# Kernel optimization log

Hardware: AMD Instinct MI355X
Metric: run time of the kernel (lower is better)

Reference implementation:

```python
import jax, jax.numpy as jnp
import numpy as np

B_SZ, L, D_MODEL = 4, 4096, 512
D_INNER, N_HEADS, HEAD_DIM = 1024, 16, 64
D_STATE, D_CONV, CHUNK = 64, 4, 64
EPS = 1e-5


def setup_inputs() -> dict:
    key = jax.random.key(0)
    ks = jax.random.split(key, 12)
    return {
        'x': jax.random.normal(ks[0], (B_SZ, L, D_MODEL), jnp.float32),
        'W_in': jax.random.normal(ks[1], (D_MODEL, 2 * D_INNER), jnp.float32) * 0.02,
        'conv_x_kernel': jax.random.normal(ks[2], (D_CONV, 1, D_INNER), jnp.float32) * 0.1,
        'conv_x_bias': jnp.zeros((D_INNER,), jnp.float32),
        'conv_z_kernel': jax.random.normal(ks[3], (D_CONV, 1, D_INNER), jnp.float32) * 0.1,
        'conv_z_bias': jnp.zeros((D_INNER,), jnp.float32),
        'W_xdbl': jax.random.normal(ks[4], (D_INNER, N_HEADS + 2 * D_STATE), jnp.float32) * 0.02,
        'dt_bias': jax.random.normal(ks[5], (N_HEADS,), jnp.float32) * 0.5,
        'A_log': jax.random.uniform(ks[6], (N_HEADS,), jnp.float32, 0.0, 1.0),
        'D': jnp.ones((N_HEADS,), jnp.float32),
        'norm_weight': jnp.ones((D_INNER,), jnp.float32),
        'W_out': jax.random.normal(ks[7], (D_INNER, D_MODEL), jnp.float32) * 0.02,
    }


def dwconv(x, kernel, bias):
    # x: (b, l, d); kernel: (k, 1, d) depthwise, flax 'SAME' padding
    out = jax.lax.conv_general_dilated(
        x, kernel, window_strides=(1,), padding='SAME',
        dimension_numbers=('NWC', 'WIO', 'NWC'),
        feature_group_count=x.shape[-1])
    return out + bias


def segsum(a):
    # stable segment-sum: out[..., d, e] = sum_{e < i <= d} a[..., i]; -inf above diag
    T = a.shape[-1]
    a_rep = jnp.broadcast_to(a[..., :, None], a.shape + (T,))
    strict = jnp.tril(jnp.ones((T, T), bool), -1)
    seg = jnp.cumsum(jnp.where(strict, a_rep, 0.0), axis=-2)
    return jnp.where(jnp.tril(jnp.ones((T, T), bool)), seg, -jnp.inf)


def ssd(x, A, B, C, chunk):
    # x: (b,l,h,p), A: (b,l,h), B/C: (b,l,n) (single group, broadcast over heads)
    b, l, h, p = x.shape
    c = l // chunk
    x = x.reshape(b, c, chunk, h, p)
    A = A.reshape(b, c, chunk, h).transpose(0, 3, 1, 2)  # (b,h,c,l)
    B = B.reshape(b, c, chunk, -1)
    C = C.reshape(b, c, chunk, -1)
    A_cum = jnp.cumsum(A, axis=-1)
    Lmat = jnp.exp(segsum(A))  # (b,h,c,l,l)
    Y_diag = jnp.einsum('bcln,bcsn,bhcls,bcshp->bclhp', C, B, Lmat, x)
    decay_states = jnp.exp(A_cum[..., -1:] - A_cum)
    states = jnp.einsum('bcln,bhcl,bclhp->bchpn', B, decay_states, x)
    states = jnp.concatenate([jnp.zeros_like(states[:, :1]), states], axis=1)
    A_last = jnp.pad(A_cum[..., -1], ((0, 0), (0, 0), (1, 0)))
    decay_chunk = jnp.exp(segsum(A_last))  # (b,h,c+1,c+1)
    new_states = jnp.einsum('bhzc,bchpn->bzhpn', decay_chunk, states)
    states, final_state = new_states[:, :-1], new_states[:, -1]
    Y_off = jnp.einsum('bcln,bchpn,bhcl->bclhp', C, states, jnp.exp(A_cum))
    Y = (Y_diag + Y_off).reshape(b, l, h, p)
    return Y, final_state


def reference(x, W_in, conv_x_kernel, conv_x_bias, conv_z_kernel, conv_z_bias,
              W_xdbl, dt_bias, A_log, D, norm_weight, W_out):
    b, l, _ = x.shape
    xz = x @ W_in
    xi, z = jnp.split(xz, 2, axis=-1)
    xi = jax.nn.silu(dwconv(xi, conv_x_kernel, conv_x_bias))
    z = jax.nn.silu(dwconv(z, conv_z_kernel, conv_z_bias))
    x_dbl = xi @ W_xdbl  # (b,l,h+2n)
    dt = x_dbl[..., :N_HEADS]
    Bmat = x_dbl[..., N_HEADS:N_HEADS + D_STATE]
    Cmat = x_dbl[..., N_HEADS + D_STATE:]
    dt = jax.nn.softplus(dt + dt_bias)  # (b,l,h)
    A = -jnp.exp(A_log)  # (h,)
    xh = xi.reshape(b, l, N_HEADS, HEAD_DIM)
    y, _ = ssd(xh * dt[..., None], A * dt, Bmat, Cmat, CHUNK)
    y = y + xh * D[..., None]
    y = y.reshape(b, l, D_INNER)
    # gated RMSNorm (Mamba2 style): gate with silu(z), then rmsnorm with weight
    y = y * jax.nn.silu(z)
    y = y * jax.lax.rsqrt(jnp.mean(y * y, axis=-1, keepdims=True) + EPS) * norm_weight
    return y @ W_out
```

## Files before the change

### kernel.cpp

```cpp
#include <hip/hip_runtime.h>
#include <hip/hip_bf16.h>
#include <cstdint>

#define B_SZn 4
#define SEQ_L 4096
#define D_MODELn 512
#define D_INNERn 1024
#define N_HEADSn 16
#define HEAD_DIMn 64
#define D_STATEn 64
#define CHUNKn 64
#define NCHUNK (SEQ_L / CHUNKn)
#define BL (B_SZn * SEQ_L)
#define XDBL_N (N_HEADSn + 2 * D_STATEn)

typedef __hip_bfloat16 bf16;
typedef __bf16 bf16x8 __attribute__((ext_vector_type(8)));
typedef float f32x4 __attribute__((ext_vector_type(4)));

__device__ __forceinline__ float silu_f(float v) {
    return v / (1.0f + expf(-v));
}
__device__ __forceinline__ float b2f(unsigned short u) {
    return __uint_as_float((unsigned)u << 16);
}
__device__ __forceinline__ unsigned short f2b(float f) {
    bf16 h = __float2bfloat16(f);
    return *(unsigned short*)&h;
}
__device__ __forceinline__ void stf(float* p, float v) { *p = v; }
__device__ __forceinline__ void stf(bf16* p, float v) { *p = __float2bfloat16(v); }

__device__ __forceinline__ float4 us4_to_f4(ushort4 u) {
    float4 f;
    f.x = b2f(u.x); f.y = b2f(u.y); f.z = b2f(u.z); f.w = b2f(u.w);
    return f;
}

__device__ __forceinline__ void async_copy16(void* lds, const void* g) {
    __builtin_amdgcn_global_load_lds(
        (const __attribute__((address_space(1))) unsigned int*)g,
        (__attribute__((address_space(3))) unsigned int*)lds, 16, 0, 0);
}

__global__ __launch_bounds__(256) void cvt_f32_bf16(
    const float* __restrict__ in, bf16* __restrict__ out) {
    const int idx = blockIdx.x * 256 + threadIdx.x;
    float4 v = *(const float4*)(in + (size_t)idx * 4);
    ushort4 o;
    o.x = f2b(v.x); o.y = f2b(v.y); o.z = f2b(v.z); o.w = f2b(v.w);
    *(ushort4*)((unsigned short*)out + (size_t)idx * 4) = o;
}

__global__ __launch_bounds__(256) void transpose_cvt(
    const float* __restrict__ in, bf16* __restrict__ out, int R, int C) {
    __shared__ float t[32][33];
    const int bc = blockIdx.x * 32, br = blockIdx.y * 32;
    const int tx = threadIdx.x & 31, ty = threadIdx.x >> 5;
#pragma unroll
    for (int i = ty; i < 32; i += 8) {
        int r = br + i, c = bc + tx;
        t[i][tx] = (r < R && c < C) ? in[(size_t)r * C + c] : 0.f;
    }
    __syncthreads();
#pragma unroll
    for (int i = ty; i < 32; i += 8) {
        int c = bc + i, r = br + tx;
        if (c < C && r < R) out[(size_t)c * R + r] = __float2bfloat16(t[tx][i]);
    }
}

template <typename TO>
__global__ __launch_bounds__(256) void gemm_mfma(
    const bf16* __restrict__ A, const bf16* __restrict__ Bt,
    TO* __restrict__ C, int M, int N, int K) {
    __shared__ __align__(16) unsigned short Al[2][128 * 32];
    __shared__ __align__(16) unsigned short Bl[2][128 * 32];
    const int tid = threadIdx.x;
    const int wave = tid >> 6, lane = tid & 63;
    const int wm = (wave >> 1) * 64, wn = (wave & 1) * 64;
    int lin = blockIdx.y * gridDim.x + blockIdx.x;
    const int nwg = gridDim.x * gridDim.y;
    if ((nwg & 7) == 0) lin = (lin & 7) * (nwg >> 3) + (lin >> 3);
    const int bm = (lin / gridDim.x) * 128, bn = (lin % gridDim.x) * 128;
    f32x4 acc[4][4];
#pragma unroll
    for (int m = 0; m < 4; ++m)
#pragma unroll
        for (int n = 0; n < 4; ++n) acc[m][n] = (f32x4)(0.f);

    const int lrow = lane & 15, lk8 = (lane >> 4) * 8;
    const int srow = tid >> 2, sc8 = (tid & 3) * 8;
    for (int k0 = 0; k0 < K; k0 += 64) {
#pragma unroll
        for (int h = 0; h < 2; ++h) {
            const int kh = k0 + h * 32;
            async_copy16((char*)&Al[h][0] + (size_t)(wave * 64) * 16,
                         A + (size_t)(bm + srow) * K + kh + sc8);
            async_copy16((char*)&Al[h][0] + (size_t)(256 + wave * 64) * 16,
                         A + (size_t)(bm + 64 + srow) * K + kh + sc8);
            async_copy16((char*)&Bl[h][0] + (size_t)(wave * 64) * 16,
                         Bt + (size_t)(bn + srow) * K + kh + sc8);
            async_copy16((char*)&Bl[h][0] + (size_t)(256 + wave * 64) * 16,
                         Bt + (size_t)(bn + 64 + srow) * K + kh + sc8);
        }
        __syncthreads();
#pragma unroll
        for (int h = 0; h < 2; ++h) {
            bf16x8 af[4], bfr[4];
#pragma unroll
            for (int m = 0; m < 4; ++m)
                af[m] = *(const bf16x8*)(&Al[h][(wm + m * 16 + lrow) * 32 + lk8]);
#pragma unroll
            for (int n = 0; n < 4; ++n)
                bfr[n] = *(const bf16x8*)(&Bl[h][(wn + n * 16 + lrow) * 32 + lk8]);
#pragma unroll
            for (int m = 0; m < 4; ++m)
#pragma unroll
                for (int n = 0; n < 4; ++n)
                    acc[m][n] = __builtin_amdgcn_mfma_f32_16x16x32_bf16(
                        af[m], bfr[n], acc[m][n], 0, 0, 0);
        }
        __syncthreads();
    }
#pragma unroll
    for (int m = 0; m < 4; ++m) {
#pragma unroll
        for (int n = 0; n < 4; ++n) {
#pragma unroll
            for (int r = 0; r < 4; ++r) {
                int row = bm + wm + m * 16 + (lane >> 4) * 4 + r;
                int col = bn + wn + n * 16 + (lane & 15);
                if (row < M && col < N)
                    stf(&C[(size_t)row * N + col], acc[m][n][r]);
            }
        }
    }
}

__global__ __launch_bounds__(256) void conv_silu_kernel(
    const bf16* __restrict__ xz,
    const float* __restrict__ kx, const float* __restrict__ bx,
    const float* __restrict__ kz, const float* __restrict__ bz,
    bf16* __restrict__ xi, bf16* __restrict__ zo) {
    const int tid = threadIdx.x;
    const int d4 = tid * 4;
    const int blk = blockIdx.x;
    const int l0 = (blk * 8) & (SEQ_L - 1);
    const int b = (blk * 8) >> 12;
    const unsigned short* base = (const unsigned short*)xz +
                                 ((size_t)b * SEQ_L) * (2 * D_INNERn);
    float4 wx[4], wz[4];
#pragma unroll
    for (int k = 0; k < 4; ++k) {
        wx[k] = *(const float4*)(kx + k * D_INNERn + d4);
        wz[k] = *(const float4*)(kz + k * D_INNERn + d4);
    }
    const float4 bxv = *(const float4*)(bx + d4);
    const float4 bzv = *(const float4*)(bz + d4);
    float4 vx[4], vz[4];
#pragma unroll
    for (int j = 0; j < 3; ++j) {
        int l = l0 - 1 + j;
        if (l >= 0) {
            const unsigned short* row = base + (size_t)l * (2 * D_INNERn);
            vx[j] = us4_to_f4(*(const ushort4*)(row + d4));
            vz[j] = us4_to_f4(*(const ushort4*)(row + D_INNERn + d4));
        } else {
            vx[j] = make_float4(0.f, 0.f, 0.f, 0.f);
            vz[j] = make_float4(0.f, 0.f, 0.f, 0.f);
        }
    }
    unsigned short* xout = (unsigned short*)xi;
    unsigned short* zout = (unsigned short*)zo;
#pragma unroll
    for (int j = 0; j < 8; ++j) {
        const int lread = l0 + 2 + j;
        if (lread < SEQ_L) {
            const unsigned short* row = base + (size_t)lread * (2 * D_INNERn);
            vx[3] = us4_to_f4(*(const ushort4*)(row + d4));
            vz[3] = us4_to_f4(*(const ushort4*)(row + D_INNERn + d4));
        } else {
            vx[3] = make_float4(0.f, 0.f, 0.f, 0.f);
            vz[3] = make_float4(0.f, 0.f, 0.f, 0.f);
        }
        float4 ax = bxv, az = bzv;
#pragma unroll
        for (int k = 0; k < 4; ++k) {
            ax.x += vx[k].x * wx[k].x; ax.y += vx[k].y * wx[k].y;
            ax.z += vx[k].z * wx[k].z; ax.w += vx[k].w * wx[k].w;
            az.x += vz[k].x * wz[k].x; az.y += vz[k].y * wz[k].y;
            az.z += vz[k].z * wz[k].z; az.w += vz[k].w * wz[k].w;
        }
        ushort4 ox, oz;
        ox.x = f2b(silu_f(ax.x)); ox.y = f2b(silu_f(ax.y));
        ox.z = f2b(silu_f(ax.z)); ox.w = f2b(silu_f(ax.w));
        oz.x = f2b(silu_f(az.x)); oz.y = f2b(silu_f(az.y));
        oz.z = f2b(silu_f(az.z)); oz.w = f2b(silu_f(az.w));
        const size_t obase = ((size_t)b * SEQ_L + l0 + j) * D_INNERn + d4;
        *(ushort4*)(xout + obase) = ox;
        *(ushort4*)(zout + obase) = oz;
        vx[0] = vx[1]; vx[1] = vx[2]; vx[2] = vx[3];
        vz[0] = vz[1]; vz[1] = vz[2]; vz[2] = vz[3];
    }
}

__global__ __launch_bounds__(256) void dt_kernel(
    const unsigned short* __restrict__ xdbl, const float* __restrict__ dt_bias,
    float* __restrict__ dtp) {
    const int idx = blockIdx.x * 256 + threadIdx.x;
    const int h = idx & 15;
    const int r = idx >> 4;
    float v = b2f(xdbl[(size_t)r * XDBL_N + h]) + dt_bias[h];
    dtp[idx] = (v > 20.f) ? v : log1pf(expf(v));
}

__global__ __launch_bounds__(256) void ssd_chunk_mfma(
    const unsigned short* __restrict__ xdbl, const bf16* __restrict__ xi,
    const float* __restrict__ dtp, const float* __restrict__ A_log,
    const float* __restrict__ Dvec,
    unsigned short* __restrict__ y, unsigned short* __restrict__ S,
    float* __restrict__ acum_g, float* __restrict__ rchunk) {
    __shared__ __align__(16) unsigned short sBb[64 * 72];
    __shared__ __align__(16) unsigned short sCb[64 * 72];
    __shared__ __align__(16) unsigned short sXT[64 * 72];
    __shared__ __align__(16) unsigned short sGb[64 * 72];
    __shared__ __align__(16) unsigned short sWB[64 * 72];
    __shared__ float sdtp[64], sacum[64], sw[64];
    const int bid = blockIdx.x;
    const int h = bid & 15;
    const int bc = bid >> 4;
    const int c = bc & (NCHUNK - 1);
    const int b = bc >> 6;
    const int tid = threadIdx.x;
    const int wave = tid >> 6, lane = tid & 63;
    const int lrow = lane & 15, lk8 = (lane >> 4) * 8;
    const int row0 = b * SEQ_L + c * CHUNKn;
    const float Ah = -expf(A_log[h]);
    const float Dh = Dvec[h];

    if (tid < 64) sdtp[tid] = dtp[(size_t)(row0 + tid) * N_HEADSn + h];
    const unsigned short* xius = (const unsigned short*)xi;
#pragma unroll
    for (int it = 0; it < 16; ++it) {
        int e = tid + it * 256;
        int s = e >> 6, n = e & 63;
        const unsigned short* xr = xdbl + (size_t)(row0 + s) * XDBL_N + N_HEADSn;
        sBb[s * 72 + n] = xr[n];
        sCb[s * 72 + n] = xr[D_STATEn + n];
        sXT[n * 72 + s] = xius[(size_t)(row0 + s) * D_INNERn + h * HEAD_DIMn + n];
    }
    __syncthreads();
    if (wave == 0) {
        float v = Ah * sdtp[lane];
#pragma unroll
        for (int o = 1; o < 64; o <<= 1) {
            float t = __shfl_up(v, o);
            if (lane >= o) v += t;
        }
        sacum[lane] = v;
        float last = __shfl(v, 63);
        sw[lane] = expf(last - v) * sdtp[lane];
        acum_g[(size_t)bid * 64 + lane] = v;
        if (lane == 63) rchunk[bid] = expf(v);
    }
    f32x4 acc1[4];
#pragma unroll
    for (int t = 0; t < 4; ++t) acc1[t] = (f32x4)(0.f);
#pragma unroll
    for (int ks = 0; ks < 2; ++ks) {
        bf16x8 a = *(const bf16x8*)(&sCb[(wave * 16 + lrow) * 72 + ks * 32 + lk8]);
#pragma unroll
        for (int t = 0; t < 4; ++t) {
            bf16x8 bb = *(const bf16x8*)(&sBb[(t * 16 + lrow) * 72 + ks * 32 + lk8]);
            acc1[t] = __builtin_amdgcn_mfma_f32_16x16x32_bf16(a, bb, acc1[t], 0, 0, 0);
        }
    }
    __syncthreads();
#pragma unroll
    for (int t = 0; t < 4; ++t) {
#pragma unroll
        for (int r = 0; r < 4; ++r) {
            int l = wave * 16 + (lane >> 4) * 4 + r;
            int s = t * 16 + lrow;
            float val = 0.f;
            if (l >= s) val = acc1[t][r] * expf(sacum[l] - sacum[s]) * sdtp[s];
            sGb[l * 72 + s] = f2b(val);
        }
    }
#pragma unroll
    for (int it = 0; it < 16; ++it) {
        int e = tid + it * 256;
        int s = e >> 6, n = e & 63;
        sWB[n * 72 + s] = f2b(sw[s] * b2f(sBb[s * 72 + n]));
    }
    __syncthreads();
    f32x4 acc2[4], acc3[4];
#pragma unroll
    for (int t = 0; t < 4; ++t) { acc2[t] = (f32x4)(0.f); acc3[t] = (f32x4)(0.f); }
#pragma unroll
    for (int ks = 0; ks < 2; ++ks) {
        bf16x8 a2 = *(const bf16x8*)(&sGb[(wave * 16 + lrow) * 72 + ks * 32 + lk8]);
        bf16x8 a3 = *(const bf16x8*)(&sXT[(wave * 16 + lrow) * 72 + ks * 32 + lk8]);
#pragma unroll
        for (int t = 0; t < 4; ++t) {
            bf16x8 b2v = *(const bf16x8*)(&sXT[(t * 16 + lrow) * 72 + ks * 32 + lk8]);
            bf16x8 b3v = *(const bf16x8*)(&sWB[(t * 16 + lrow) * 72 + ks * 32 + lk8]);
            acc2[t] = __builtin_amdgcn_mfma_f32_16x16x32_bf16(a2, b2v, acc2[t], 0, 0, 0);
            acc3[t] = __builtin_amdgcn_mfma_f32_16x16x32_bf16(a3, b3v, acc3[t], 0, 0, 0);
        }
    }
#pragma unroll
    for (int t = 0; t < 4; ++t) {
#pragma unroll
        for (int r = 0; r < 4; ++r) {
            int rr = wave * 16 + (lane >> 4) * 4 + r;
            int cc = t * 16 + lrow;
            float xv = b2f(sXT[cc * 72 + rr]);
            y[(size_t)(row0 + rr) * D_INNERn + h * HEAD_DIMn + cc] =
                f2b(acc2[t][r] + Dh * xv);
            S[(size_t)bid * 4096 + rr * 64 + cc] = f2b(acc3[t][r]);
        }
    }
}

__global__ __launch_bounds__(256) void chunk_scan_kernel(
    unsigned short* __restrict__ S, const float* __restrict__ rchunk) {
    const int idx = blockIdx.x * 256 + threadIdx.x;
    const int pn2 = (idx & 2047) * 2;
    const int bh = idx >> 11;
    const int h = bh & 15;
    const int b = bh >> 4;
    float P0 = 0.f, P1 = 0.f;
    for (int c = 0; c < NCHUNK; ++c) {
        int bid = (b * NCHUNK + c) * N_HEADSn + h;
        size_t off = (size_t)bid * 4096 + pn2;
        unsigned int v = *(unsigned int*)(S + off);
        float s0 = b2f((unsigned short)(v & 0xffff));
        float s1 = b2f((unsigned short)(v >> 16));
        *(unsigned int*)(S + off) =
            (unsigned int)f2b(P0) | ((unsigned int)f2b(P1) << 16);
        float rc = rchunk[bid];
        P0 = rc * P0 + s0;
        P1 = rc * P1 + s1;
    }
}

__global__ __launch_bounds__(256) void yoff_mfma(
    const unsigned short* __restrict__ xdbl, const unsigned short* __restrict__ S,
    const float* __restrict__ acum_g, unsigned short* __restrict__ y) {
    __shared__ __align__(16) unsigned short sCb[64 * 72];
    __shared__ __align__(16) unsigned short sP[64 * 72];
    __shared__ float se[64];
    const int bid = blockIdx.x;
    const int h = bid & 15;
    const int bc = bid >> 4;
    const int c = bc & (NCHUNK - 1);
    const int b = bc >> 6;
    const int tid = threadIdx.x;
    const int wave = tid >> 6, lane = tid & 63;
    const int lrow = lane & 15, lk8 = (lane >> 4) * 8;
    const int row0 = b * SEQ_L + c * CHUNKn;
    if (tid < 64) se[tid] = expf(acum_g[(size_t)bid * 64 + tid]);
#pragma unroll
    for (int it = 0; it < 16; ++it) {
        int e = tid + it * 256;
        int r = e >> 6, n = e & 63;
        sCb[r * 72 + n] = xdbl[(size_t)(row0 + r) * XDBL_N + N_HEADSn + D_STATEn + n];
        sP[r * 72 + n] = S[(size_t)bid * 4096 + e];
    }
    __syncthreads();
    f32x4 acc[4];
#pragma unroll
    for (int t = 0; t < 4; ++t) acc[t] = (f32x4)(0.f);
#pragma unroll
    for (int ks = 0; ks < 2; ++ks) {
        bf16x8 a = *(const bf16x8*)(&sCb[(wave * 16 + lrow) * 72 + ks * 32 + lk8]);
#pragma unroll
        for (int t = 0; t < 4; ++t) {
            bf16x8 bb = *(const bf16x8*)(&sP[(t * 16 + lrow) * 72 + ks * 32 + lk8]);
            acc[t] = __builtin_amdgcn_mfma_f32_16x16x32_bf16(a, bb, acc[t], 0, 0, 0);
        }
    }
#pragma unroll
    for (int t = 0; t < 4; ++t) {
#pragma unroll
        for (int r = 0; r < 4; ++r) {
            int l = wave * 16 + (lane >> 4) * 4 + r;
            int p = t * 16 + lrow;
            size_t idx = (size_t)(row0 + l) * D_INNERn + h * HEAD_DIMn + p;
            y[idx] = f2b(b2f(y[idx]) + acc[t][r] * se[l]);
        }
    }
}

__global__ __launch_bounds__(256) void gate_norm_kernel(
    const unsigned short* __restrict__ y, const bf16* __restrict__ zb,
    const float* __restrict__ nw, bf16* __restrict__ y_bf) {
    const int row = blockIdx.x;
    const int tid = threadIdx.x;
    const size_t base = (size_t)row * D_INNERn + tid * 4;
    ushort4 yu = *(const ushort4*)(y + base);
    ushort4 zu = *(const ushort4*)((const unsigned short*)zb + base);
    float v0 = b2f(yu.x) * silu_f(b2f(zu.x));
    float v1 = b2f(yu.y) * silu_f(b2f(zu.y));
    float v2 = b2f(yu.z) * silu_f(b2f(zu.z));
    float v3 = b2f(yu.w) * silu_f(b2f(zu.w));
    float ss = v0 * v0 + v1 * v1 + v2 * v2 + v3 * v3;
#pragma unroll
    for (int o = 32; o > 0; o >>= 1) ss += __shfl_xor(ss, o);
    __shared__ float sred[4];
    if ((tid & 63) == 0) sred[tid >> 6] = ss;
    __syncthreads();
    float total = sred[0] + sred[1] + sred[2] + sred[3];
    float scale = rsqrtf(total * (1.0f / D_INNERn) + 1e-5f);
    float4 wv = *(const float4*)(nw + tid * 4);
    ushort4 o4;
    o4.x = f2b(v0 * scale * wv.x);
    o4.y = f2b(v1 * scale * wv.y);
    o4.z = f2b(v2 * scale * wv.z);
    o4.w = f2b(v3 * scale * wv.w);
    *(ushort4*)((unsigned short*)y_bf + base) = o4;
}

extern "C" void kernel_launch(void* const* d_in, const int* in_sizes, int n_in,
                              void* d_out, int out_size, void* d_ws, size_t ws_size,
                              hipStream_t stream) {
    (void)in_sizes; (void)n_in; (void)out_size; (void)ws_size;
    const float* x       = (const float*)d_in[0];
    const float* W_in    = (const float*)d_in[1];
    const float* ckx     = (const float*)d_in[2];
    const float* cbx     = (const float*)d_in[3];
    const float* ckz     = (const float*)d_in[4];
    const float* cbz     = (const float*)d_in[5];
    const float* W_xdbl  = (const float*)d_in[6];
    const float* dt_bias = (const float*)d_in[7];
    const float* A_log   = (const float*)d_in[8];
    const float* Dvec    = (const float*)d_in[9];
    const float* nw      = (const float*)d_in[10];
    const float* W_out   = (const float*)d_in[11];
    float* out = (float*)d_out;
    char* w = (char*)d_ws;

    bf16*  xz     = (bf16*)(w);
    unsigned short* y = (unsigned short*)(w);
    bf16*  xi     = (bf16*)(w + 67108864);
    bf16*  zb     = (bf16*)(w + 100663296);
    char*  Sreg   = w + 134217728;
    unsigned short* S = (unsigned short*)Sreg;
    bf16*  x_bf   = (bf16*)Sreg;
    bf16*  W_in_T = (bf16*)(Sreg + 16777216);
    bf16*  W_xd_T = (bf16*)(Sreg + 18874368);
    bf16*  y_bf   = (bf16*)Sreg;
    bf16*  W_o_T  = (bf16*)(Sreg + 33554432);
    unsigned short* xdbl = (unsigned short*)(w + 201326592);
    float* dtp    = (float*)(w + 210763776);
    float* acum   = (float*)(w + 211812352);
    float* rchunk = (float*)(w + 212860928);

    cvt_f32_bf16<<<BL * D_MODELn / 1024, 256, 0, stream>>>(x, x_bf);
    transpose_cvt<<<dim3(2048 / 32, 512 / 32), 256, 0, stream>>>(W_in, W_in_T, 512, 2048);
    transpose_cvt<<<dim3(5, 1024 / 32), 256, 0, stream>>>(W_xdbl, W_xd_T, 1024, 144);
    gemm_mfma<bf16><<<dim3(2048 / 128, BL / 128), 256, 0, stream>>>(
        x_bf, W_in_T, xz, BL, 2048, D_MODELn);
    conv_silu_kernel<<<BL / 8, 256, 0, stream>>>(xz, ckx, cbx, ckz, cbz, xi, zb);
    gemm_mfma<bf16><<<dim3(2, BL / 128), 256, 0, stream>>>(
        xi, W_xd_T, (bf16*)xdbl, BL, XDBL_N, D_INNERn);
    dt_kernel<<<BL * N_HEADSn / 256, 256, 0, stream>>>(xdbl, dt_bias, dtp);
    ssd_chunk_mfma<<<B_SZn * NCHUNK * N_HEADSn, 256, 0, stream>>>(
        xdbl, xi, dtp, A_log, Dvec, y, S, acum, rchunk);
    chunk_scan_kernel<<<B_SZn * N_HEADSn * 2048 / 256, 256, 0, stream>>>(S, rchunk);
    yoff_mfma<<<B_SZn * NCHUNK * N_HEADSn, 256, 0, stream>>>(xdbl, S, acum, y);
    transpose_cvt<<<dim3(512 / 32, 1024 / 32), 256, 0, stream>>>(W_out, W_o_T, 1024, 512);
    gate_norm_kernel<<<BL, 256, 0, stream>>>(y, zb, nw, y_bf);
    gemm_mfma<float><<<dim3(512 / 128, BL / 128), 256, 0, stream>>>(
        y_bf, W_o_T, out, BL, D_MODELn, D_INNERn);
}
```

Before: 257.8 us.

## Add wide 128x256 GEMM for in-proj, fuse dt softplus into SSD, set MFMA priority

The input projection GEMM switches to a new 512-thread kernel with 128x256 tiles, a grouped block-order remap and two-stage K staging. This is meant to improve B-tile reuse and L2 locality. The separate dt softplus kernel is removed and its work is recomputed inside ssd_chunk_mfma, which saves a launch and the dtp round trip through memory. s_setprio is raised around the MFMA loops in the SSD kernels so matrix work gets scheduling priority. The wider tile means fewer workgroups and more registers per wave, which may reduce occupancy.

```diff
diff --git a/kernel.cpp b/kernel.cpp
--- a/kernel.cpp
+++ b/kernel.cpp
@@ -138,6 +138,72 @@
     }
 }
 
+template <typename TO>
+__global__ __launch_bounds__(512) void gemm_mfma_wide(
+    const bf16* __restrict__ A, const bf16* __restrict__ Bt,
+    TO* __restrict__ C, int M, int N, int K) {
+    __shared__ __align__(16) unsigned short Al[2][128 * 32];
+    __shared__ __align__(16) unsigned short Bl[2][256 * 32];
+    const int tid = threadIdx.x;
+    const int wave = tid >> 6, lane = tid & 63;
+    const int wm = (wave >> 2) * 64, wn = (wave & 3) * 64;
+    int lin = blockIdx.y * gridDim.x + blockIdx.x;
+    const int nwg = gridDim.x * gridDim.y;
+    if ((nwg & 7) == 0) lin = (lin & 7) * (nwg >> 3) + (lin >> 3);
+    const int bm = (lin / gridDim.x) * 128, bn = (lin % gridDim.x) * 256;
+    f32x4 acc[4][4];
+#pragma unroll
+    for (int m = 0; m < 4; ++m)
+#pragma unroll
+        for (int n = 0; n < 4; ++n) acc[m][n] = (f32x4)(0.f);
+
+    const int lrow = lane & 15, lk8 = (lane >> 4) * 8;
+    const int srow = tid >> 2, sc8 = (tid & 3) * 8;
+    for (int k0 = 0; k0 < K; k0 += 64) {
+#pragma unroll
+        for (int h = 0; h < 2; ++h) {
+            const int kh = k0 + h * 32;
+            async_copy16((char*)&Al[h][0] + (size_t)(wave * 64) * 16,
+                         A + (size_t)(bm + srow) * K + kh + sc8);
+            async_copy16((char*)&Bl[h][0] + (size_t)(wave * 64) * 16,
+                         Bt + (size_t)(bn + srow) * K + kh + sc8);
+            async_copy16((char*)&Bl[h][0] + (size_t)(512 + wave * 64) * 16,
+                         Bt + (size_t)(bn + 128 + srow) * K + kh + sc8);
+        }
+        __syncthreads();
+#pragma unroll
+        for (int h = 0; h < 2; ++h) {
+            bf16x8 af[4], bfr[4];
+#pragma unroll
+            for (int m = 0; m < 4; ++m)
+                af[m] = *(const bf16x8*)(&Al[h][(wm + m * 16 + lrow) * 32 + lk8]);
+#pragma unroll
+            for (int n = 0; n < 4; ++n)
+                bfr[n] = *(const bf16x8*)(&Bl[h][(wn + n * 16 + lrow) * 32 + lk8]);
+#pragma unroll
+            for (int m = 0; m < 4; ++m)
+#pragma unroll
+                for (int n = 0; n < 4; ++n)
+                    acc[m][n] = __builtin_amdgcn_mfma_f32_16x16x32_bf16(
+                        af[m], bfr[n], acc[m][n], 0, 0, 0);
+        }
+        __syncthreads();
+    }
+#pragma unroll
+    for (int m = 0; m < 4; ++m) {
+#pragma unroll
+        for (int n = 0; n < 4; ++n) {
+#pragma unroll
+            for (int r = 0; r < 4; ++r) {
+                int row = bm + wm + m * 16 + (lane >> 4) * 4 + r;
+                int col = bn + wn + n * 16 + (lane & 15);
+                if (row < M && col < N)
+                    stf(&C[(size_t)row * N + col], acc[m][n][r]);
+            }
+        }
+    }
+}
+
 __global__ __launch_bounds__(256) void conv_silu_kernel(
     const bf16* __restrict__ xz,
     const float* __restrict__ kx, const float* __restrict__ bx,
@@ -205,19 +271,9 @@
     }
 }
 
-__global__ __launch_bounds__(256) void dt_kernel(
-    const unsigned short* __restrict__ xdbl, const float* __restrict__ dt_bias,
-    float* __restrict__ dtp) {
-    const int idx = blockIdx.x * 256 + threadIdx.x;
-    const int h = idx & 15;
-    const int r = idx >> 4;
-    float v = b2f(xdbl[(size_t)r * XDBL_N + h]) + dt_bias[h];
-    dtp[idx] = (v > 20.f) ? v : log1pf(expf(v));
-}
-
 __global__ __launch_bounds__(256) void ssd_chunk_mfma(
     const unsigned short* __restrict__ xdbl, const bf16* __restrict__ xi,
-    const float* __restrict__ dtp, const float* __restrict__ A_log,
+    const float* __restrict__ dt_bias, const float* __restrict__ A_log,
     const float* __restrict__ Dvec,
     unsigned short* __restrict__ y, unsigned short* __restrict__ S,
     float* __restrict__ acum_g, float* __restrict__ rchunk) {
@@ -239,7 +295,10 @@
     const float Ah = -expf(A_log[h]);
     const float Dh = Dvec[h];
 
-    if (tid < 64) sdtp[tid] = dtp[(size_t)(row0 + tid) * N_HEADSn + h];
+    if (tid < 64) {
+        float v = b2f(xdbl[(size_t)(row0 + tid) * XDBL_N + h]) + dt_bias[h];
+        sdtp[tid] = (v > 20.f) ? v : log1pf(expf(v));
+    }
     const unsigned short* xius = (const unsigned short*)xi;
 #pragma unroll
     for (int it = 0; it < 16; ++it) {
@@ -267,6 +326,7 @@
     f32x4 acc1[4];
 #pragma unroll
     for (int t = 0; t < 4; ++t) acc1[t] = (f32x4)(0.f);
+    __builtin_amdgcn_s_setprio(1);
 #pragma unroll
     for (int ks = 0; ks < 2; ++ks) {
         bf16x8 a = *(const bf16x8*)(&sCb[(wave * 16 + lrow) * 72 + ks * 32 + lk8]);
@@ -276,6 +336,7 @@
             acc1[t] = __builtin_amdgcn_mfma_f32_16x16x32_bf16(a, bb, acc1[t], 0, 0, 0);
         }
     }
+    __builtin_amdgcn_s_setprio(0);
     __syncthreads();
 #pragma unroll
     for (int t = 0; t < 4; ++t) {
@@ -298,6 +359,7 @@
     f32x4 acc2[4], acc3[4];
 #pragma unroll
     for (int t = 0; t < 4; ++t) { acc2[t] = (f32x4)(0.f); acc3[t] = (f32x4)(0.f); }
+    __builtin_amdgcn_s_setprio(1);
 #pragma unroll
     for (int ks = 0; ks < 2; ++ks) {
         bf16x8 a2 = *(const bf16x8*)(&sGb[(wave * 16 + lrow) * 72 + ks * 32 + lk8]);
@@ -310,6 +372,7 @@
             acc3[t] = __builtin_amdgcn_mfma_f32_16x16x32_bf16(a3, b3v, acc3[t], 0, 0, 0);
         }
     }
+    __builtin_amdgcn_s_setprio(0);
 #pragma unroll
     for (int t = 0; t < 4; ++t) {
 #pragma unroll
@@ -373,6 +436,7 @@
     f32x4 acc[4];
 #pragma unroll
     for (int t = 0; t < 4; ++t) acc[t] = (f32x4)(0.f);
+    __builtin_amdgcn_s_setprio(1);
 #pragma unroll
     for (int ks = 0; ks < 2; ++ks) {
         bf16x8 a = *(const bf16x8*)(&sCb[(wave * 16 + lrow) * 72 + ks * 32 + lk8]);
@@ -382,6 +446,7 @@
             acc[t] = __builtin_amdgcn_mfma_f32_16x16x32_bf16(a, bb, acc[t], 0, 0, 0);
         }
     }
+    __builtin_amdgcn_s_setprio(0);
 #pragma unroll
     for (int t = 0; t < 4; ++t) {
 #pragma unroll
@@ -454,21 +519,19 @@
     bf16*  y_bf   = (bf16*)Sreg;
     bf16*  W_o_T  = (bf16*)(Sreg + 33554432);
     unsigned short* xdbl = (unsigned short*)(w + 201326592);
-    float* dtp    = (float*)(w + 210763776);
     float* acum   = (float*)(w + 211812352);
     float* rchunk = (float*)(w + 212860928);
 
     cvt_f32_bf16<<<BL * D_MODELn / 1024, 256, 0, stream>>>(x, x_bf);
     transpose_cvt<<<dim3(2048 / 32, 512 / 32), 256, 0, stream>>>(W_in, W_in_T, 512, 2048);
     transpose_cvt<<<dim3(5, 1024 / 32), 256, 0, stream>>>(W_xdbl, W_xd_T, 1024, 144);
-    gemm_mfma<bf16><<<dim3(2048 / 128, BL / 128), 256, 0, stream>>>(
+    gemm_mfma_wide<bf16><<<dim3(2048 / 256, BL / 128), 512, 0, stream>>>(
         x_bf, W_in_T, xz, BL, 2048, D_MODELn);
     conv_silu_kernel<<<BL / 8, 256, 0, stream>>>(xz, ckx, cbx, ckz, cbz, xi, zb);
     gemm_mfma<bf16><<<dim3(2, BL / 128), 256, 0, stream>>>(
         xi, W_xd_T, (bf16*)xdbl, BL, XDBL_N, D_INNERn);
-    dt_kernel<<<BL * N_HEADSn / 256, 256, 0, stream>>>(xdbl, dt_bias, dtp);
     ssd_chunk_mfma<<<B_SZn * NCHUNK * N_HEADSn, 256, 0, stream>>>(
-        xdbl, xi, dtp, A_log, Dvec, y, S, acum, rchunk);
+        xdbl, xi, dt_bias, A_log, Dvec, y, S, acum, rchunk);
     chunk_scan_kernel<<<B_SZn * N_HEADSn * 2048 / 256, 256, 0, stream>>>(S, rchunk);
     yoff_mfma<<<B_SZn * NCHUNK * N_HEADSn, 256, 0, stream>>>(xdbl, S, acum, y);
     transpose_cvt<<<dim3(512 / 32, 1024 / 32), 256, 0, stream>>>(W_out, W_o_T, 1024, 512);
```

Measured after the change: 241.9 us. -6.2%, faster.
